# Optimization experiments

Hardware: AMD Instinct MI355X
Metric: run time of the kernel (lower is better)

Reference implementation:

```python
import jax, jax.numpy as jnp
import numpy as np

D = 1024   # model dim
H = 16     # heads
HD = D // H
L = 14     # layers
FF = 4096  # ffn hidden
T = 768    # sequence length


def layer_norm(x, g, b, eps):
    m = x.mean(-1, keepdims=True)
    v = ((x - m) ** 2).mean(-1, keepdims=True)
    return (x - m) / jnp.sqrt(v + eps) * g + b


def rel_pos_emb(t, d):
    # EspnetRelPositionalEncoding: concat(flip(pe_positive), pe_negative[1:]) -> (1, 2t-1, d)
    pos = jnp.arange(t, dtype=jnp.float32)
    div = jnp.exp(jnp.arange(0, d, 2, dtype=jnp.float32) * (-jnp.log(10000.0) / d))
    ang = pos[:, None] * div[None, :]                              # (t, d/2)
    pe_pos = jnp.stack([jnp.sin(ang), jnp.cos(ang)], -1).reshape(t, d)
    pe_neg = jnp.stack([jnp.sin(-ang), jnp.cos(-ang)], -1).reshape(t, d)
    return jnp.concatenate([pe_pos[::-1], pe_neg[1:]], 0)[None]    # (1, 2t-1, d)


def rel_shift(x):
    # x: (b, h, t, 2t-1) -> (b, h, t, t), Transformer-XL shift
    b, h, t, n = x.shape
    xp = jnp.concatenate([jnp.zeros((b, h, t, 1), x.dtype), x], -1)  # (b,h,t,n+1)
    xp = xp.reshape(b, h, n + 1, t)
    x = xp[:, :, 1:].reshape(b, h, t, n)
    return x[..., : n // 2 + 1]


def setup_inputs() -> dict:
    key = jax.random.key(0)
    ks = iter(jax.random.split(key, 40))
    s = 0.02
    nrm = lambda k, shape: jax.random.normal(k, shape, dtype=jnp.float32) * s
    return {
        "xs": jax.random.normal(next(ks), (1, T, D), dtype=jnp.float32),
        "embed_W": nrm(next(ks), (D, D)), "embed_b": jnp.zeros((D,), jnp.float32),
        "embed_ln_g": jnp.ones((D,), jnp.float32), "embed_ln_b": jnp.zeros((D,), jnp.float32),
        "Wq": nrm(next(ks), (L, D, D)), "bq": jnp.zeros((L, D), jnp.float32),
        "Wk": nrm(next(ks), (L, D, D)), "bk": jnp.zeros((L, D), jnp.float32),
        "Wv": nrm(next(ks), (L, D, D)), "bv": jnp.zeros((L, D), jnp.float32),
        "Wo": nrm(next(ks), (L, D, D)), "bo": jnp.zeros((L, D), jnp.float32),
        "Wp": nrm(next(ks), (L, D, D)),
        "pos_u": nrm(next(ks), (L, H, HD)), "pos_v": nrm(next(ks), (L, H, HD)),
        "ln1_g": jnp.ones((L, D), jnp.float32), "ln1_b": jnp.zeros((L, D), jnp.float32),
        "ln2_g": jnp.ones((L, D), jnp.float32), "ln2_b": jnp.zeros((L, D), jnp.float32),
        "ff_W1": nrm(next(ks), (L, D, FF)), "ff_b1": jnp.zeros((L, FF), jnp.float32),
        "ff_W2": nrm(next(ks), (L, FF, D)), "ff_b2": jnp.zeros((L, D), jnp.float32),
        "after_g": jnp.ones((D,), jnp.float32), "after_b": jnp.zeros((D,), jnp.float32),
    }


def reference(xs, embed_W, embed_b, embed_ln_g, embed_ln_b,
              Wq, bq, Wk, bk, Wv, bv, Wo, bo, Wp, pos_u, pos_v,
              ln1_g, ln1_b, ln2_g, ln2_b, ff_W1, ff_b1, ff_W2, ff_b2,
              after_g, after_b):
    b, t, _ = xs.shape
    # LegacyLinearNoSubsampling: Linear -> LayerNorm(eps=1e-5) -> (dropout) -> ReLU
    h = jnp.maximum(layer_norm(xs @ embed_W + embed_b, embed_ln_g, embed_ln_b, 1e-5), 0.0)
    x = h * jnp.sqrt(jnp.float32(D))          # pos-enc scale factor
    pos = rel_pos_emb(t, D)                    # (1, 2t-1, D)
    scale = jnp.float32(HD) ** -0.5
    for i in range(L):
        res = x
        xn = layer_norm(x, ln1_g[i], ln1_b[i], 1e-12)
        q = (xn @ Wq[i] + bq[i]).reshape(b, t, H, HD).transpose(0, 2, 1, 3)   # bhtd
        k = (xn @ Wk[i] + bk[i]).reshape(b, t, H, HD).transpose(0, 2, 1, 3)
        v = (xn @ Wv[i] + bv[i]).reshape(b, t, H, HD).transpose(0, 2, 1, 3)
        p = (pos @ Wp[i]).reshape(1, 2 * t - 1, H, HD).transpose(0, 2, 1, 3)  # bhnd
        ac = jnp.einsum('bhtd,bhsd->bhts', q + pos_u[i][None, :, None, :], k)
        bd = rel_shift(jnp.einsum('bhtd,bhnd->bhtn', q + pos_v[i][None, :, None, :], p))
        attn = jax.nn.softmax((ac + bd) * scale, axis=-1)
        o = jnp.einsum('bhts,bhsd->bhtd', attn, v).transpose(0, 2, 1, 3).reshape(b, t, D)
        x = res + (o @ Wo[i] + bo[i])
        res = x
        xn = layer_norm(x, ln2_g[i], ln2_b[i], 1e-12)
        x = res + (jnp.maximum(xn @ ff_W1[i] + ff_b1[i], 0.0) @ ff_W2[i] + ff_b2[i])
    return layer_norm(x, after_g, after_b, 1e-5)
```

## Files before the change

### kernel.cpp

```cpp
#include <hip/hip_runtime.h>
#include <hip/hip_bf16.h>
#include <math.h>

#define D_    1024
#define H_    16
#define HD_   64
#define L_    14
#define FF_   4096
#define T_    768
#define NPOS_ (2*T_-1)

using s16x8 = __attribute__((ext_vector_type(8))) short;
using f32x4 = __attribute__((ext_vector_type(4))) float;

__device__ inline short f2bf(float f) {
  __hip_bfloat16 h = __float2bfloat16(f);
  return *reinterpret_cast<short*>(&h);
}
__device__ inline float bf2f(unsigned short u) {
  union { unsigned u; float f; } v; v.u = ((unsigned)u) << 16; return v.f;
}

__device__ inline void gload_lds16(const unsigned short* g, short* lds) {
  __builtin_amdgcn_global_load_lds(
      (const __attribute__((address_space(1))) unsigned int*)g,
      (__attribute__((address_space(3))) unsigned int*)lds,
      16, 0, 0);
}

__device__ inline float waveRedSum(float v) {
#pragma unroll
  for (int o = 32; o > 0; o >>= 1) v += __shfl_down(v, o, 64);
  return v;
}
__device__ inline float blockRedSum(float v, float* sh) {
  int lane = threadIdx.x & 63, wid = threadIdx.x >> 6;
  v = waveRedSum(v);
  if (lane == 0) sh[wid] = v;
  __syncthreads();
  if (wid == 0) {
    float x = (lane < 4) ? sh[lane] : 0.f;
    x = waveRedSum(x);
    if (lane == 0) sh[0] = x;
  }
  __syncthreads();
  float r = sh[0];
  __syncthreads();
  return r;
}

__global__ __launch_bounds__(256) void ln_kernel(
    const float* __restrict__ x, const float* __restrict__ g,
    const float* __restrict__ b, void* __restrict__ y,
    float eps, int relu, float scale, int obf)
{
  __shared__ float sh[8];
  long row = blockIdx.x;
  const float* xr = x + row * D_;
  int tid = threadIdx.x;
  float4 v = *(const float4*)&xr[tid * 4];
  float s  = v.x + v.y + v.z + v.w;
  float sq = v.x * v.x + v.y * v.y + v.z * v.z + v.w * v.w;
  float mean = blockRedSum(s, sh) * (1.f / D_);
  float esq  = blockRedSum(sq, sh) * (1.f / D_);
  float var  = esq - mean * mean;
  if (var < 0.f) var = 0.f;
  float inv = rsqrtf(var + eps);
  float4 gv = *(const float4*)&g[tid * 4];
  float4 bv = *(const float4*)&b[tid * 4];
  float o0 = (v.x - mean) * inv * gv.x + bv.x;
  float o1 = (v.y - mean) * inv * gv.y + bv.y;
  float o2 = (v.z - mean) * inv * gv.z + bv.z;
  float o3 = (v.w - mean) * inv * gv.w + bv.w;
  if (relu) {
    o0 = fmaxf(o0, 0.f); o1 = fmaxf(o1, 0.f);
    o2 = fmaxf(o2, 0.f); o3 = fmaxf(o3, 0.f);
  }
  o0 *= scale; o1 *= scale; o2 *= scale; o3 *= scale;
  if (obf) {
    short4 sv;
    sv.x = f2bf(o0); sv.y = f2bf(o1); sv.z = f2bf(o2); sv.w = f2bf(o3);
    *(short4*)&((unsigned short*)y)[row * D_ + tid * 4] = sv;
  } else {
    float4 ov; ov.x = o0; ov.y = o1; ov.z = o2; ov.w = o3;
    *(float4*)&((float*)y)[row * D_ + tid * 4] = ov;
  }
}

__global__ __launch_bounds__(256) void transpose_kernel(
    const float* __restrict__ in, unsigned short* __restrict__ out, int K, int N)
{
  __shared__ unsigned short t[32][33];
  long z = blockIdx.z;
  in  += z * (long)K * N;
  out += z * (long)K * N;
  int n0 = blockIdx.x * 32, k0 = blockIdx.y * 32;
  int tid = threadIdx.x;
  int r = tid >> 3, c4 = (tid & 7) * 4;
  float4 v = *(const float4*)&in[(long)(k0 + r) * N + n0 + c4];
  t[r][c4 + 0] = (unsigned short)f2bf(v.x);
  t[r][c4 + 1] = (unsigned short)f2bf(v.y);
  t[r][c4 + 2] = (unsigned short)f2bf(v.z);
  t[r][c4 + 3] = (unsigned short)f2bf(v.w);
  __syncthreads();
  ushort4 s;
  s.x = t[c4 + 0][r]; s.y = t[c4 + 1][r]; s.z = t[c4 + 2][r]; s.w = t[c4 + 3][r];
  *(ushort4*)&out[(long)(n0 + r) * K + k0 + c4] = s;
}

template<int BM, int BN, int BMODE, bool CBF16>
__global__ __launch_bounds__(256) void gemm5_kernel(
    const unsigned short* __restrict__ A, int lda, long sAz,
    const void* __restrict__ B0, const void* __restrict__ B1, const void* __restrict__ B2,
    int ldb, long sBz,
    void* C0, void* C1, void* C2, int ldc, long sCz,
    const float* __restrict__ bias0, const float* __restrict__ bias1,
    const float* __restrict__ bias2,
    const float* __restrict__ resid, int ldres,
    int M, int N, int K, int zPerG, int relu, int nM)
{
  constexpr int FM = BM / 32, FN = BN / 32;
  constexpr int A_IT = BM / 32;
  constexpr int B_IT = BN / 32;
  constexpr int NSH = (BN == 128) ? 7 : 6;

  __shared__ short As[BM * 64];
  __shared__ short Bs[BN * 64];

  int nb = gridDim.x, bid = blockIdx.x;
  int q = nb >> 3, r = nb & 7, xcd = bid & 7, idx = bid >> 3;
  int lbid = (xcd < r ? xcd * (q + 1) : r * (q + 1) + (xcd - r) * q) + idx;
  int mT = lbid % nM, nT = lbid / nM;
  int m0 = mT * BM, n0 = nT * BN;

  int z = blockIdx.z;
  int g = z / zPerG, zb = z - g * zPerG;
  A += (long)zb * sAz;
  const void* Bv = (g == 0) ? B0 : ((g == 1) ? B1 : B2);
  void* Cv       = (g == 0) ? C0 : ((g == 1) ? C1 : C2);
  const float* bias = (g == 0) ? bias0 : ((g == 1) ? bias1 : bias2);
  const float* Bf = (const float*)Bv + zb * sBz;
  const unsigned short* Bh = (const unsigned short*)Bv + zb * sBz;
  float* Cf = (float*)Cv + zb * sCz;
  unsigned short* Ch = (unsigned short*)Cv + zb * sCz;

  int tid = threadIdx.x, lane = tid & 63, wid = tid >> 6;
  int wm0 = (wid >> 1) * (BM / 2), wn0 = (wid & 1) * (BN / 2);
  int lr = lane & 15, kl = (lane >> 4) * 8;

  f32x4 acc[FM][FN];
#pragma unroll
  for (int i = 0; i < FM; ++i)
#pragma unroll
    for (int j = 0; j < FN; ++j)
#pragma unroll
      for (int rr = 0; rr < 4; ++rr) acc[i][j][rr] = 0.f;

  for (int k0 = 0; k0 < K; k0 += 64) {
    if constexpr (BMODE == 1) {
      int lrow8 = lane >> 3;
      int lc8 = lane & 7;
#pragma unroll
      for (int it = 0; it < A_IT; ++it) {
        int row0 = (wid + it * 4) * 8;
        int row = row0 + lrow8;
        int gcol = lc8 ^ (row & 7);
        gload_lds16(A + (long)(m0 + row) * lda + k0 + gcol * 8, &As[row0 * 64]);
      }
#pragma unroll
      for (int it = 0; it < B_IT; ++it) {
        int row0 = (wid + it * 4) * 8;
        int row = row0 + lrow8;
        int gcol = lc8 ^ (row & 7);
        gload_lds16(Bh + (long)(n0 + row) * ldb + k0 + gcol * 8, &Bs[row0 * 64]);
      }
    } else {
#pragma unroll
      for (int it = 0; it < A_IT; ++it) {
        int f = tid + it * 256;
        int row = f >> 3, c8 = f & 7;
        int gm = m0 + row;
        s16x8 v = {0, 0, 0, 0, 0, 0, 0, 0};
        if (gm < M) v = *(const s16x8*)(A + (long)gm * lda + k0 + c8 * 8);
        *(s16x8*)&As[row * 64 + ((c8 ^ (row & 7)) << 3)] = v;
      }
      constexpr int B_IT2 = BN / 16;
#pragma unroll
      for (int it = 0; it < B_IT2; ++it) {
        int p = tid + it * 256;
        int n = p & (BN - 1), kq = p >> NSH;
        int gn = n0 + n;
        const float* bp = Bf + (long)(k0 + kq * 4) * ldb + gn;
        short4 s;
        s.x = f2bf(bp[0]); s.y = f2bf(bp[ldb]);
        s.z = f2bf(bp[2 * (long)ldb]); s.w = f2bf(bp[3 * (long)ldb]);
        *(short4*)&Bs[n * 64 + ((kq << 2) ^ ((n & 7) << 3))] = s;
      }
    }
    __syncthreads();
#pragma unroll
    for (int kk = 0; kk < 2; ++kk) {
      s16x8 a[FM], b[FN];
#pragma unroll
      for (int i = 0; i < FM; ++i) {
        int row = wm0 + i * 16 + lr;
        a[i] = *(const s16x8*)&As[row * 64 + ((kk * 32 + kl) ^ ((lr & 7) << 3))];
      }
#pragma unroll
      for (int j = 0; j < FN; ++j) {
        int row = wn0 + j * 16 + lr;
        b[j] = *(const s16x8*)&Bs[row * 64 + ((kk * 32 + kl) ^ ((lr & 7) << 3))];
      }
#pragma unroll
      for (int i = 0; i < FM; ++i)
#pragma unroll
        for (int j = 0; j < FN; ++j)
          acc[i][j] = __builtin_amdgcn_mfma_f32_16x16x32_bf16(a[i], b[j], acc[i][j], 0, 0, 0);
    }
    __syncthreads();
  }
#pragma unroll
  for (int i = 0; i < FM; ++i) {
#pragma unroll
    for (int j = 0; j < FN; ++j) {
      int n = n0 + wn0 + j * 16 + lr;
      float bv = bias ? bias[n] : 0.f;
#pragma unroll
      for (int rr = 0; rr < 4; ++rr) {
        int m = m0 + wm0 + i * 16 + (lane >> 4) * 4 + rr;
        if (m < M) {
          float v = acc[i][j][rr] + bv;
          if (resid) v += resid[(long)m * ldres + n];
          if (relu)  v = fmaxf(v, 0.f);
          if constexpr (CBF16) Ch[(long)m * ldc + n] = (unsigned short)f2bf(v);
          else                 Cf[(long)m * ldc + n] = v;
        }
      }
    }
  }
}

__global__ __launch_bounds__(256) void f2bf_kernel(
    const float* __restrict__ x, unsigned short* __restrict__ y, int n4)
{
  int i = blockIdx.x * 256 + threadIdx.x;
  if (i >= n4) return;
  float4 v = *(const float4*)&x[i * 4];
  short4 s; s.x = f2bf(v.x); s.y = f2bf(v.y); s.z = f2bf(v.z); s.w = f2bf(v.w);
  *(short4*)&y[i * 4] = s;
}

__global__ __launch_bounds__(256) void pos_kernel(unsigned short* __restrict__ pos)
{
  int idx = blockIdx.x * 256 + threadIdx.x;
  if (idx >= NPOS_ * (D_ / 2)) return;
  int n = idx / (D_ / 2), i = idx % (D_ / 2);
  float r = (float)(T_ - 1 - n);
  float div = __expf((float)(2 * i) * (-logf(10000.f) / (float)D_));
  float ang = r * div;
  pos[(long)n * D_ + 2 * i]     = (unsigned short)f2bf(sinf(ang));
  pos[(long)n * D_ + 2 * i + 1] = (unsigned short)f2bf(cosf(ang));
}

__global__ __launch_bounds__(256) void flash_attn_kernel(
    const unsigned short* __restrict__ Q, const unsigned short* __restrict__ K,
    const unsigned short* __restrict__ V, const unsigned short* __restrict__ P,
    const float* __restrict__ posu, const float* __restrict__ posv,
    unsigned short* __restrict__ O)
{
  __shared__ short Ks[64 * 64];
  __shared__ short Vs[64 * 64];
  __shared__ short Ps[96 * 64];
  __shared__ float Grgn[32 * 99];
  __shared__ float mxls[2][32], smls[2][32];

  short* qu = (short*)Grgn;
  short* qv = qu + 32 * 64;
  float* G  = Grgn;
  short* Pf = (short*)Grgn;

  int h = blockIdx.y;
  int t0 = blockIdx.x * 32;
  int tid = threadIdx.x, lane = tid & 63, w = tid >> 6;
  int wr = w >> 1, wc = w & 1;
  int lr = lane & 15, lg = lane >> 4;
  int kl = lg * 8;
  const float* pu = posu + h * HD_;
  const float* pv = posv + h * HD_;

  {
    int row = tid >> 3, c8 = tid & 7;
    s16x8 q8 = *(const s16x8*)(Q + (long)(t0 + row) * D_ + h * HD_ + c8 * 8);
    const unsigned short* qp = (const unsigned short*)&q8;
    s16x8 su, sv;
#pragma unroll
    for (int j = 0; j < 8; ++j) {
      float qf = bf2f(qp[j]);
      su[j] = f2bf(qf + pu[c8 * 8 + j]);
      sv[j] = f2bf(qf + pv[c8 * 8 + j]);
    }
    int sw = row * 64 + ((c8 ^ (row & 7)) << 3);
    *(s16x8*)&qu[sw] = su;
    *(s16x8*)&qv[sw] = sv;
  }
  __syncthreads();
  s16x8 aqu[2], aqv[2];
#pragma unroll
  for (int kk = 0; kk < 2; ++kk) {
    int row = wr * 16 + lr;
    int col = (kk * 32 + kl) ^ ((lr & 7) << 3);
    aqu[kk] = *(const s16x8*)&qu[row * 64 + col];
    aqv[kk] = *(const s16x8*)&qv[row * 64 + col];
  }

  float m_[4], l_[4];
  f32x4 acc_o[2];
#pragma unroll
  for (int rr = 0; rr < 4; ++rr) { m_[rr] = -1e30f; l_[rr] = 0.f; }
#pragma unroll
  for (int j = 0; j < 2; ++j)
#pragma unroll
    for (int rr = 0; rr < 4; ++rr) acc_o[j][rr] = 0.f;

  int lrow8 = lane >> 3, lc8 = lane & 7;

  for (int s0 = 0; s0 < T_; s0 += 64) {
    int base = s0 - t0 + T_ - 32;
    __syncthreads();
#pragma unroll
    for (int it = 0; it < 2; ++it) {
      int row0 = (w + it * 4) * 8;
      int row = row0 + lrow8;
      int gcol = lc8 ^ (row & 7);
      gload_lds16(K + (long)(s0 + row) * D_ + h * HD_ + gcol * 8, &Ks[row0 * 64]);
    }
#pragma unroll
    for (int it = 0; it < 4; ++it) {
      int d = tid & 63, sq = tid >> 6;
      int s = it * 16 + sq * 4;
      const unsigned short* vp = V + (long)(s0 + s) * D_ + h * HD_ + d;
      short4 sv4;
      sv4.x = (short)vp[0];
      sv4.y = (short)vp[D_];
      sv4.z = (short)vp[2 * D_];
      sv4.w = (short)vp[3 * D_];
      *(short4*)&Vs[d * 64 + (s ^ ((d & 7) << 3))] = sv4;
    }
#pragma unroll
    for (int it = 0; it < 3; ++it) {
      int row0 = (w + it * 4) * 8;
      int row = row0 + lrow8;
      int gp = base + row; if (gp > NPOS_ - 1) gp = NPOS_ - 1;
      int gcol = lc8 ^ (row & 7);
      gload_lds16(P + (long)gp * D_ + h * HD_ + gcol * 8, &Ps[row0 * 64]);
    }
    __syncthreads();
    f32x4 a_ac[2], a_g[3];
#pragma unroll
    for (int j = 0; j < 2; ++j)
#pragma unroll
      for (int rr = 0; rr < 4; ++rr) a_ac[j][rr] = 0.f;
#pragma unroll
    for (int j = 0; j < 3; ++j)
#pragma unroll
      for (int rr = 0; rr < 4; ++rr) a_g[j][rr] = 0.f;
#pragma unroll
    for (int j = 0; j < 2; ++j)
#pragma unroll
      for (int kk = 0; kk < 2; ++kk) {
        int row = wc * 32 + j * 16 + lr;
        s16x8 b = *(const s16x8*)&Ks[row * 64 + ((kk * 32 + kl) ^ ((lr & 7) << 3))];
        a_ac[j] = __builtin_amdgcn_mfma_f32_16x16x32_bf16(aqu[kk], b, a_ac[j], 0, 0, 0);
      }
#pragma unroll
    for (int j = 0; j < 3; ++j)
#pragma unroll
      for (int kk = 0; kk < 2; ++kk) {
        int row = wc * 48 + j * 16 + lr;
        s16x8 b = *(const s16x8*)&Ps[row * 64 + ((kk * 32 + kl) ^ ((lr & 7) << 3))];
        a_g[j] = __builtin_amdgcn_mfma_f32_16x16x32_bf16(aqv[kk], b, a_g[j], 0, 0, 0);
      }
#pragma unroll
    for (int j = 0; j < 3; ++j)
#pragma unroll
      for (int rr = 0; rr < 4; ++rr) {
        int row = wr * 16 + lg * 4 + rr;
        int col = wc * 48 + j * 16 + lr;
        G[row * 99 + col] = a_g[j][rr];
      }
    __syncthreads();
    float sreg[2][4], pm[4];
#pragma unroll
    for (int rr = 0; rr < 4; ++rr) {
      int row = wr * 16 + lg * 4 + rr;
#pragma unroll
      for (int j = 0; j < 2; ++j) {
        int c = wc * 32 + j * 16 + lr;
        int gc = c - row + 31;
        sreg[j][rr] = (a_ac[j][rr] + G[row * 99 + gc]) * 0.125f;
      }
      pm[rr] = fmaxf(sreg[0][rr], sreg[1][rr]);
    }
#pragma unroll
    for (int o = 1; o < 16; o <<= 1)
#pragma unroll
      for (int rr = 0; rr < 4; ++rr) pm[rr] = fmaxf(pm[rr], __shfl_xor(pm[rr], o, 64));
    if (lr == 0) {
#pragma unroll
      for (int rr = 0; rr < 4; ++rr) mxls[wc][wr * 16 + lg * 4 + rr] = pm[rr];
    }
    __syncthreads();
    float ps[4];
#pragma unroll
    for (int rr = 0; rr < 4; ++rr) {
      int row = wr * 16 + lg * 4 + rr;
      float mnew = fmaxf(m_[rr], fmaxf(mxls[0][row], mxls[1][row]));
      float sc = __expf(m_[rr] - mnew);
      m_[rr] = mnew;
      l_[rr] *= sc;
      acc_o[0][rr] *= sc;
      acc_o[1][rr] *= sc;
      float p0 = __expf(sreg[0][rr] - mnew);
      float p1 = __expf(sreg[1][rr] - mnew);
      ps[rr] = p0 + p1;
      int c0 = wc * 32 + lr, c1 = wc * 32 + 16 + lr;
      ((unsigned short*)Pf)[row * 64 + (c0 ^ ((row & 7) << 3))] = (unsigned short)f2bf(p0);
      ((unsigned short*)Pf)[row * 64 + (c1 ^ ((row & 7) << 3))] = (unsigned short)f2bf(p1);
    }
#pragma unroll
    for (int o = 1; o < 16; o <<= 1)
#pragma unroll
      for (int rr = 0; rr < 4; ++rr) ps[rr] += __shfl_xor(ps[rr], o, 64);
    if (lr == 0) {
#pragma unroll
      for (int rr = 0; rr < 4; ++rr) smls[wc][wr * 16 + lg * 4 + rr] = ps[rr];
    }
    __syncthreads();
#pragma unroll
    for (int rr = 0; rr < 4; ++rr) {
      int row = wr * 16 + lg * 4 + rr;
      l_[rr] += smls[0][row] + smls[1][row];
    }
    s16x8 ap[2];
#pragma unroll
    for (int kk = 0; kk < 2; ++kk) {
      int row = wr * 16 + lr;
      ap[kk] = *(const s16x8*)&((unsigned short*)Pf)[row * 64 + ((kk * 32 + kl) ^ ((lr & 7) << 3))];
    }
#pragma unroll
    for (int j = 0; j < 2; ++j)
#pragma unroll
      for (int kk = 0; kk < 2; ++kk) {
        int row = wc * 32 + j * 16 + lr;
        s16x8 b = *(const s16x8*)&Vs[row * 64 + ((kk * 32 + kl) ^ ((lr & 7) << 3))];
        acc_o[j] = __builtin_amdgcn_mfma_f32_16x16x32_bf16(ap[kk], b, acc_o[j], 0, 0, 0);
      }
  }
#pragma unroll
  for (int j = 0; j < 2; ++j)
#pragma unroll
    for (int rr = 0; rr < 4; ++rr) {
      int row = t0 + wr * 16 + lg * 4 + rr;
      int col = h * HD_ + wc * 32 + j * 16 + lr;
      O[(long)row * D_ + col] = (unsigned short)f2bf(acc_o[j][rr] / l_[rr]);
    }
}

extern "C" void kernel_launch(void* const* d_in, const int* in_sizes, int n_in,
                              void* d_out, int out_size, void* d_ws, size_t ws_size,
                              hipStream_t stream) {
  const float* xs       = (const float*)d_in[0];
  const float* embed_W  = (const float*)d_in[1];
  const float* embed_b  = (const float*)d_in[2];
  const float* embed_g  = (const float*)d_in[3];
  const float* embed_bt = (const float*)d_in[4];
  const float* Wq = (const float*)d_in[5];
  const float* bq = (const float*)d_in[6];
  const float* Wk = (const float*)d_in[7];
  const float* bk = (const float*)d_in[8];
  const float* Wv = (const float*)d_in[9];
  const float* bv = (const float*)d_in[10];
  const float* Wo = (const float*)d_in[11];
  const float* bo = (const float*)d_in[12];
  const float* Wp = (const float*)d_in[13];
  const float* pos_u = (const float*)d_in[14];
  const float* pos_v = (const float*)d_in[15];
  const float* ln1_g = (const float*)d_in[16];
  const float* ln1_b = (const float*)d_in[17];
  const float* ln2_g = (const float*)d_in[18];
  const float* ln2_b = (const float*)d_in[19];
  const float* ff_W1 = (const float*)d_in[20];
  const float* ff_b1 = (const float*)d_in[21];
  const float* ff_W2 = (const float*)d_in[22];
  const float* ff_b2 = (const float*)d_in[23];
  const float* after_g = (const float*)d_in[24];
  const float* after_b = (const float*)d_in[25];
  float* out = (float*)d_out;

  char* w = (char*)d_ws;
  auto carve = [&](size_t bytes) { char* p = w; w += (bytes + 255) & ~(size_t)255; return p; };
  float* bufX  = (float*)carve((size_t)T_ * D_ * 4);
  float* bufT  = (float*)carve((size_t)T_ * D_ * 4);
  unsigned short* xsb  = (unsigned short*)carve((size_t)T_ * D_ * 2);
  unsigned short* XNb  = (unsigned short*)carve((size_t)T_ * D_ * 2);
  unsigned short* Qb   = (unsigned short*)carve((size_t)T_ * D_ * 2);
  unsigned short* Kb   = (unsigned short*)carve((size_t)T_ * D_ * 2);
  unsigned short* Vb   = (unsigned short*)carve((size_t)T_ * D_ * 2);
  unsigned short* Ob   = (unsigned short*)carve((size_t)T_ * D_ * 2);
  unsigned short* Hb   = (unsigned short*)carve((size_t)T_ * FF_ * 2);
  unsigned short* posT = (unsigned short*)carve((size_t)(NPOS_ + 8) * D_ * 2);
  unsigned short* Pall = (unsigned short*)carve((size_t)L_ * NPOS_ * D_ * 2);
  size_t szDD = (size_t)D_ * D_;
  unsigned short* embedWt = (unsigned short*)carve(szDD * 2);
  unsigned short* WqT = (unsigned short*)carve((size_t)L_ * szDD * 2);
  unsigned short* WkT = (unsigned short*)carve((size_t)L_ * szDD * 2);
  unsigned short* WvT = (unsigned short*)carve((size_t)L_ * szDD * 2);
  unsigned short* WoT = (unsigned short*)carve((size_t)L_ * szDD * 2);
  unsigned short* WpT = (unsigned short*)carve((size_t)L_ * szDD * 2);
  unsigned short* W1T = (unsigned short*)carve((size_t)L_ * D_ * FF_ * 2);
  unsigned short* W2T = (unsigned short*)carve((size_t)L_ * D_ * FF_ * 2);
  bool fast = ((size_t)(w - (char*)d_ws) <= ws_size);

  {
    int n = NPOS_ * (D_ / 2);
    pos_kernel<<<(n + 255) / 256, 256, 0, stream>>>(posT);
  }
  f2bf_kernel<<<(T_ * D_ / 4 + 255) / 256, 256, 0, stream>>>(xs, xsb, T_ * D_ / 4);

  if (fast) {
    transpose_kernel<<<dim3(32, 32, 1),  256, 0, stream>>>(embed_W, embedWt, D_, D_);
    transpose_kernel<<<dim3(32, 32, L_), 256, 0, stream>>>(Wq, WqT, D_, D_);
    transpose_kernel<<<dim3(32, 32, L_), 256, 0, stream>>>(Wk, WkT, D_, D_);
    transpose_kernel<<<dim3(32, 32, L_), 256, 0, stream>>>(Wv, WvT, D_, D_);
    transpose_kernel<<<dim3(32, 32, L_), 256, 0, stream>>>(Wo, WoT, D_, D_);
    transpose_kernel<<<dim3(32, 32, L_), 256, 0, stream>>>(Wp, WpT, D_, D_);
    transpose_kernel<<<dim3(128, 32, L_), 256, 0, stream>>>(ff_W1, W1T, D_, FF_);
    transpose_kernel<<<dim3(32, 128, L_), 256, 0, stream>>>(ff_W2, W2T, FF_, D_);

    gemm5_kernel<32, 128, 1, false><<<dim3(192, 1, 1), 256, 0, stream>>>(
        xsb, D_, 0, embedWt, nullptr, nullptr, D_, 0,
        bufT, nullptr, nullptr, D_, 0, embed_b, nullptr, nullptr,
        nullptr, 0, T_, D_, D_, 1, 0, 24);
    ln_kernel<<<T_, 256, 0, stream>>>(bufT, embed_g, embed_bt, bufX, 1e-5f, 1, 32.0f, 0);

    gemm5_kernel<128, 64, 1, true><<<dim3(192, 1, 14), 256, 0, stream>>>(
        posT, D_, 0, WpT, nullptr, nullptr, D_, (long)szDD,
        Pall, nullptr, nullptr, D_, (long)NPOS_ * D_, nullptr, nullptr, nullptr,
        nullptr, 0, NPOS_, D_, D_, 14, 0, 12);

    for (int i = 0; i < L_; ++i) {
      ln_kernel<<<T_, 256, 0, stream>>>(bufX, ln1_g + (long)i * D_, ln1_b + (long)i * D_,
                                        XNb, 1e-12f, 0, 1.0f, 1);
      gemm5_kernel<32, 128, 1, true><<<dim3(192, 1, 3), 256, 0, stream>>>(
          XNb, D_, 0, WqT + i * szDD, WkT + i * szDD, WvT + i * szDD, D_, 0,
          Qb, Kb, Vb, D_, 0,
          bq + (long)i * D_, bk + (long)i * D_, bv + (long)i * D_,
          nullptr, 0, T_, D_, D_, 1, 0, 24);
      flash_attn_kernel<<<dim3(T_ / 32, H_), 256, 0, stream>>>(
          Qb, Kb, Vb, Pall + (long)i * NPOS_ * D_,
          pos_u + (long)i * D_, pos_v + (long)i * D_, Ob);
      gemm5_kernel<32, 64, 1, false><<<dim3(384, 1, 1), 256, 0, stream>>>(
          Ob, D_, 0, WoT + i * szDD, nullptr, nullptr, D_, 0,
          bufX, nullptr, nullptr, D_, 0, bo + (long)i * D_, nullptr, nullptr,
          bufX, D_, T_, D_, D_, 1, 0, 24);
      ln_kernel<<<T_, 256, 0, stream>>>(bufX, ln2_g + (long)i * D_, ln2_b + (long)i * D_,
                                        XNb, 1e-12f, 0, 1.0f, 1);
      gemm5_kernel<32, 128, 1, true><<<dim3(768, 1, 1), 256, 0, stream>>>(
          XNb, D_, 0, W1T + (size_t)i * D_ * FF_, nullptr, nullptr, D_, 0,
          Hb, nullptr, nullptr, FF_, 0, ff_b1 + (long)i * FF_, nullptr, nullptr,
          nullptr, 0, T_, FF_, D_, 1, 1, 24);
      gemm5_kernel<32, 64, 1, false><<<dim3(384, 1, 1), 256, 0, stream>>>(
          Hb, FF_, 0, W2T + (size_t)i * D_ * FF_, nullptr, nullptr, FF_, 0,
          bufX, nullptr, nullptr, D_, 0, ff_b2 + (long)i * D_, nullptr, nullptr,
          bufX, D_, T_, FF_, FF_, 1, 0, 24);
    }
  } else {
    gemm5_kernel<32, 128, 0, false><<<dim3(192, 1, 1), 256, 0, stream>>>(
        xsb, D_, 0, embed_W, nullptr, nullptr, D_, 0,
        bufT, nullptr, nullptr, D_, 0, embed_b, nullptr, nullptr,
        nullptr, 0, T_, D_, D_, 1, 0, 24);
    ln_kernel<<<T_, 256, 0, stream>>>(bufT, embed_g, embed_bt, bufX, 1e-5f, 1, 32.0f, 0);

    gemm5_kernel<128, 64, 0, true><<<dim3(192, 1, 14), 256, 0, stream>>>(
        posT, D_, 0, Wp, nullptr, nullptr, D_, (long)szDD,
        Pall, nullptr, nullptr, D_, (long)NPOS_ * D_, nullptr, nullptr, nullptr,
        nullptr, 0, NPOS_, D_, D_, 14, 0, 12);

    for (int i = 0; i < L_; ++i) {
      ln_kernel<<<T_, 256, 0, stream>>>(bufX, ln1_g + (long)i * D_, ln1_b + (long)i * D_,
                                        XNb, 1e-12f, 0, 1.0f, 1);
      gemm5_kernel<32, 128, 0, true><<<dim3(192, 1, 3), 256, 0, stream>>>(
          XNb, D_, 0, Wq + i * szDD, Wk + i * szDD, Wv + i * szDD, D_, 0,
          Qb, Kb, Vb, D_, 0,
          bq + (long)i * D_, bk + (long)i * D_, bv + (long)i * D_,
          nullptr, 0, T_, D_, D_, 1, 0, 24);
      flash_attn_kernel<<<dim3(T_ / 32, H_), 256, 0, stream>>>(
          Qb, Kb, Vb, Pall + (long)i * NPOS_ * D_,
          pos_u + (long)i * D_, pos_v + (long)i * D_, Ob);
      gemm5_kernel<32, 64, 0, false><<<dim3(384, 1, 1), 256, 0, stream>>>(
          Ob, D_, 0, Wo + i * szDD, nullptr, nullptr, D_, 0,
          bufX, nullptr, nullptr, D_, 0, bo + (long)i * D_, nullptr, nullptr,
          bufX, D_, T_, D_, D_, 1, 0, 24);
      ln_kernel<<<T_, 256, 0, stream>>>(bufX, ln2_g + (long)i * D_, ln2_b + (long)i * D_,
                                        XNb, 1e-12f, 0, 1.0f, 1);
      gemm5_kernel<32, 128, 0, true><<<dim3(768, 1, 1), 256, 0, stream>>>(
          XNb, D_, 0, ff_W1 + (size_t)i * D_ * FF_, nullptr, nullptr, FF_, 0,
          Hb, nullptr, nullptr, FF_, 0, ff_b1 + (long)i * FF_, nullptr, nullptr,
          nullptr, 0, T_, FF_, D_, 1, 1, 24);
      gemm5_kernel<32, 64, 0, false><<<dim3(384, 1, 1), 256, 0, stream>>>(
          Hb, FF_, 0, ff_W2 + (size_t)i * D_ * FF_, nullptr, nullptr, D_, 0,
          bufX, nullptr, nullptr, D_, 0, ff_b2 + (long)i * D_, nullptr, nullptr,
          bufX, D_, T_, FF_, FF_, 1, 0, 24);
    }
  }

  ln_kernel<<<T_, 256, 0, stream>>>(bufX, after_g, after_b, out, 1e-5f, 0, 1.0f, 0);
}
```

Before: 2.573 ms.

## Replace LDS-staged GEMM with direct-from-global register-fragment GEMM using 16-row tiles

Adds a gemm6 kernel that skips shared memory and barriers entirely. Each wave loads its MFMA A/B fragments straight from global memory into registers, and tiles are 16x128 per block. All fast-path GEMMs are switched to it with more blocks, and the LDS-async load mode is removed from gemm5. This aims to cut LDS traffic and sync overhead and to raise parallelism for the small-M GEMMs. The cost is that A fragments are re-read by all four waves and there is no cross-wave data reuse, so more load traffic goes to cache. The pos buffer padding is also increased.

```diff
diff --git a/kernel.cpp b/kernel.cpp
--- a/kernel.cpp
+++ b/kernel.cpp
@@ -108,7 +108,97 @@
   *(ushort4*)&out[(long)(n0 + r) * K + k0 + c4] = s;
 }
 
-template<int BM, int BN, int BMODE, bool CBF16>
+template<int BM, bool CBF16>
+__global__ __launch_bounds__(256) void gemm6_kernel(
+    const unsigned short* __restrict__ A, int lda, long sAz,
+    const unsigned short* __restrict__ B0, const unsigned short* __restrict__ B1,
+    const unsigned short* __restrict__ B2, int ldb, long sBz,
+    void* C0, void* C1, void* C2, int ldc, long sCz,
+    const float* __restrict__ bias0, const float* __restrict__ bias1,
+    const float* __restrict__ bias2,
+    const float* __restrict__ resid, int ldres,
+    int M, int N, int K, int zPerG, int relu, int nM)
+{
+  constexpr int FM = BM / 16;
+  constexpr int FN = 2;
+
+  int nb = gridDim.x, bid = blockIdx.x;
+  int q = nb >> 3, r = nb & 7, xcd = bid & 7, idx = bid >> 3;
+  int lbid = (xcd < r ? xcd * (q + 1) : r * (q + 1) + (xcd - r) * q) + idx;
+  int mT = lbid % nM, nT = lbid / nM;
+  int m0 = mT * BM, n0 = nT * 128;
+
+  int z = blockIdx.z;
+  int g = z / zPerG, zb = z - g * zPerG;
+  A += (long)zb * sAz;
+  const unsigned short* Bh = ((g == 0) ? B0 : ((g == 1) ? B1 : B2)) + zb * sBz;
+  void* Cv = (g == 0) ? C0 : ((g == 1) ? C1 : C2);
+  const float* bias = (g == 0) ? bias0 : ((g == 1) ? bias1 : bias2);
+  float* Cf = (float*)Cv + zb * sCz;
+  unsigned short* Ch = (unsigned short*)Cv + zb * sCz;
+
+  int tid = threadIdx.x, lane = tid & 63, wid = tid >> 6;
+  int wn0 = wid * 32;
+  int lr = lane & 15, kl = (lane >> 4) * 8;
+
+  const unsigned short* Ap[FM];
+  const unsigned short* Bp[FN];
+#pragma unroll
+  for (int i = 0; i < FM; ++i) Ap[i] = A + (long)(m0 + i * 16 + lr) * lda + kl;
+#pragma unroll
+  for (int j = 0; j < FN; ++j) Bp[j] = Bh + (long)(n0 + wn0 + j * 16 + lr) * ldb + kl;
+
+  f32x4 acc[FM][FN];
+#pragma unroll
+  for (int i = 0; i < FM; ++i)
+#pragma unroll
+    for (int j = 0; j < FN; ++j)
+#pragma unroll
+      for (int rr = 0; rr < 4; ++rr) acc[i][j][rr] = 0.f;
+
+  for (int k0 = 0; k0 < K; k0 += 64) {
+    s16x8 a[2][FM], b[2][FN];
+#pragma unroll
+    for (int kk = 0; kk < 2; ++kk) {
+#pragma unroll
+      for (int i = 0; i < FM; ++i) a[kk][i] = *(const s16x8*)(Ap[i] + kk * 32);
+#pragma unroll
+      for (int j = 0; j < FN; ++j) b[kk][j] = *(const s16x8*)(Bp[j] + kk * 32);
+    }
+#pragma unroll
+    for (int kk = 0; kk < 2; ++kk)
+#pragma unroll
+      for (int i = 0; i < FM; ++i)
+#pragma unroll
+        for (int j = 0; j < FN; ++j)
+          acc[i][j] = __builtin_amdgcn_mfma_f32_16x16x32_bf16(a[kk][i], b[kk][j], acc[i][j], 0, 0, 0);
+#pragma unroll
+    for (int i = 0; i < FM; ++i) Ap[i] += 64;
+#pragma unroll
+    for (int j = 0; j < FN; ++j) Bp[j] += 64;
+  }
+#pragma unroll
+  for (int i = 0; i < FM; ++i) {
+#pragma unroll
+    for (int j = 0; j < FN; ++j) {
+      int n = n0 + wn0 + j * 16 + lr;
+      float bv = bias ? bias[n] : 0.f;
+#pragma unroll
+      for (int rr = 0; rr < 4; ++rr) {
+        int m = m0 + i * 16 + (lane >> 4) * 4 + rr;
+        if (m < M) {
+          float v = acc[i][j][rr] + bv;
+          if (resid) v += resid[(long)m * ldres + n];
+          if (relu)  v = fmaxf(v, 0.f);
+          if constexpr (CBF16) Ch[(long)m * ldc + n] = (unsigned short)f2bf(v);
+          else                 Cf[(long)m * ldc + n] = v;
+        }
+      }
+    }
+  }
+}
+
+template<int BM, int BN, bool CBF16>
 __global__ __launch_bounds__(256) void gemm5_kernel(
     const unsigned short* __restrict__ A, int lda, long sAz,
     const void* __restrict__ B0, const void* __restrict__ B1, const void* __restrict__ B2,
@@ -121,7 +211,6 @@
 {
   constexpr int FM = BM / 32, FN = BN / 32;
   constexpr int A_IT = BM / 32;
-  constexpr int B_IT = BN / 32;
   constexpr int NSH = (BN == 128) ? 7 : 6;
 
   __shared__ short As[BM * 64];
@@ -140,7 +229,6 @@
   void* Cv       = (g == 0) ? C0 : ((g == 1) ? C1 : C2);
   const float* bias = (g == 0) ? bias0 : ((g == 1) ? bias1 : bias2);
   const float* Bf = (const float*)Bv + zb * sBz;
-  const unsigned short* Bh = (const unsigned short*)Bv + zb * sBz;
   float* Cf = (float*)Cv + zb * sCz;
   unsigned short* Ch = (unsigned short*)Cv + zb * sCz;
 
@@ -157,45 +245,26 @@
       for (int rr = 0; rr < 4; ++rr) acc[i][j][rr] = 0.f;
 
   for (int k0 = 0; k0 < K; k0 += 64) {
-    if constexpr (BMODE == 1) {
-      int lrow8 = lane >> 3;
-      int lc8 = lane & 7;
-#pragma unroll
-      for (int it = 0; it < A_IT; ++it) {
-        int row0 = (wid + it * 4) * 8;
-        int row = row0 + lrow8;
-        int gcol = lc8 ^ (row & 7);
-        gload_lds16(A + (long)(m0 + row) * lda + k0 + gcol * 8, &As[row0 * 64]);
-      }
-#pragma unroll
-      for (int it = 0; it < B_IT; ++it) {
-        int row0 = (wid + it * 4) * 8;
-        int row = row0 + lrow8;
-        int gcol = lc8 ^ (row & 7);
-        gload_lds16(Bh + (long)(n0 + row) * ldb + k0 + gcol * 8, &Bs[row0 * 64]);
-      }
-    } else {
-#pragma unroll
-      for (int it = 0; it < A_IT; ++it) {
-        int f = tid + it * 256;
-        int row = f >> 3, c8 = f & 7;
-        int gm = m0 + row;
-        s16x8 v = {0, 0, 0, 0, 0, 0, 0, 0};
-        if (gm < M) v = *(const s16x8*)(A + (long)gm * lda + k0 + c8 * 8);
-        *(s16x8*)&As[row * 64 + ((c8 ^ (row & 7)) << 3)] = v;
-      }
-      constexpr int B_IT2 = BN / 16;
-#pragma unroll
-      for (int it = 0; it < B_IT2; ++it) {
-        int p = tid + it * 256;
-        int n = p & (BN - 1), kq = p >> NSH;
-        int gn = n0 + n;
-        const float* bp = Bf + (long)(k0 + kq * 4) * ldb + gn;
-        short4 s;
-        s.x = f2bf(bp[0]); s.y = f2bf(bp[ldb]);
-        s.z = f2bf(bp[2 * (long)ldb]); s.w = f2bf(bp[3 * (long)ldb]);
-        *(short4*)&Bs[n * 64 + ((kq << 2) ^ ((n & 7) << 3))] = s;
-      }
+#pragma unroll
+    for (int it = 0; it < A_IT; ++it) {
+      int f = tid + it * 256;
+      int row = f >> 3, c8 = f & 7;
+      int gm = m0 + row;
+      s16x8 v = {0, 0, 0, 0, 0, 0, 0, 0};
+      if (gm < M) v = *(const s16x8*)(A + (long)gm * lda + k0 + c8 * 8);
+      *(s16x8*)&As[row * 64 + ((c8 ^ (row & 7)) << 3)] = v;
+    }
+    constexpr int B_IT2 = BN / 16;
+#pragma unroll
+    for (int it = 0; it < B_IT2; ++it) {
+      int p = tid + it * 256;
+      int n = p & (BN - 1), kq = p >> NSH;
+      int gn = n0 + n;
+      const float* bp = Bf + (long)(k0 + kq * 4) * ldb + gn;
+      short4 s;
+      s.x = f2bf(bp[0]); s.y = f2bf(bp[ldb]);
+      s.z = f2bf(bp[2 * (long)ldb]); s.w = f2bf(bp[3 * (long)ldb]);
+      *(short4*)&Bs[n * 64 + ((kq << 2) ^ ((n & 7) << 3))] = s;
     }
     __syncthreads();
 #pragma unroll
@@ -508,7 +577,7 @@
   unsigned short* Vb   = (unsigned short*)carve((size_t)T_ * D_ * 2);
   unsigned short* Ob   = (unsigned short*)carve((size_t)T_ * D_ * 2);
   unsigned short* Hb   = (unsigned short*)carve((size_t)T_ * FF_ * 2);
-  unsigned short* posT = (unsigned short*)carve((size_t)(NPOS_ + 8) * D_ * 2);
+  unsigned short* posT = (unsigned short*)carve((size_t)(NPOS_ + 16) * D_ * 2);
   unsigned short* Pall = (unsigned short*)carve((size_t)L_ * NPOS_ * D_ * 2);
   size_t szDD = (size_t)D_ * D_;
   unsigned short* embedWt = (unsigned short*)carve(szDD * 2);
@@ -537,51 +606,51 @@
     transpose_kernel<<<dim3(128, 32, L_), 256, 0, stream>>>(ff_W1, W1T, D_, FF_);
     transpose_kernel<<<dim3(32, 128, L_), 256, 0, stream>>>(ff_W2, W2T, FF_, D_);
 
-    gemm5_kernel<32, 128, 1, false><<<dim3(192, 1, 1), 256, 0, stream>>>(
+    gemm6_kernel<16, false><<<dim3(384, 1, 1), 256, 0, stream>>>(
         xsb, D_, 0, embedWt, nullptr, nullptr, D_, 0,
         bufT, nullptr, nullptr, D_, 0, embed_b, nullptr, nullptr,
-        nullptr, 0, T_, D_, D_, 1, 0, 24);
+        nullptr, 0, T_, D_, D_, 1, 0, 48);
     ln_kernel<<<T_, 256, 0, stream>>>(bufT, embed_g, embed_bt, bufX, 1e-5f, 1, 32.0f, 0);
 
-    gemm5_kernel<128, 64, 1, true><<<dim3(192, 1, 14), 256, 0, stream>>>(
+    gemm6_kernel<16, true><<<dim3(768, 1, 14), 256, 0, stream>>>(
         posT, D_, 0, WpT, nullptr, nullptr, D_, (long)szDD,
         Pall, nullptr, nullptr, D_, (long)NPOS_ * D_, nullptr, nullptr, nullptr,
-        nullptr, 0, NPOS_, D_, D_, 14, 0, 12);
+        nullptr, 0, NPOS_, D_, D_, 14, 0, 96);
 
     for (int i = 0; i < L_; ++i) {
       ln_kernel<<<T_, 256, 0, stream>>>(bufX, ln1_g + (long)i * D_, ln1_b + (long)i * D_,
                                         XNb, 1e-12f, 0, 1.0f, 1);
-      gemm5_kernel<32, 128, 1, true><<<dim3(192, 1, 3), 256, 0, stream>>>(
+      gemm6_kernel<16, true><<<dim3(384, 1, 3), 256, 0, stream>>>(
           XNb, D_, 0, WqT + i * szDD, WkT + i * szDD, WvT + i * szDD, D_, 0,
           Qb, Kb, Vb, D_, 0,
           bq + (long)i * D_, bk + (long)i * D_, bv + (long)i * D_,
-          nullptr, 0, T_, D_, D_, 1, 0, 24);
+          nullptr, 0, T_, D_, D_, 1, 0, 48);
       flash_attn_kernel<<<dim3(T_ / 32, H_), 256, 0, stream>>>(
           Qb, Kb, Vb, Pall + (long)i * NPOS_ * D_,
           pos_u + (long)i * D_, pos_v + (long)i * D_, Ob);
-      gemm5_kernel<32, 64, 1, false><<<dim3(384, 1, 1), 256, 0, stream>>>(
+      gemm6_kernel<16, false><<<dim3(384, 1, 1), 256, 0, stream>>>(
           Ob, D_, 0, WoT + i * szDD, nullptr, nullptr, D_, 0,
           bufX, nullptr, nullptr, D_, 0, bo + (long)i * D_, nullptr, nullptr,
-          bufX, D_, T_, D_, D_, 1, 0, 24);
+          bufX, D_, T_, D_, D_, 1, 0, 48);
       ln_kernel<<<T_, 256, 0, stream>>>(bufX, ln2_g + (long)i * D_, ln2_b + (long)i * D_,
                                         XNb, 1e-12f, 0, 1.0f, 1);
-      gemm5_kernel<32, 128, 1, true><<<dim3(768, 1, 1), 256, 0, stream>>>(
+      gemm6_kernel<16, true><<<dim3(1536, 1, 1), 256, 0, stream>>>(
           XNb, D_, 0, W1T + (size_t)i * D_ * FF_, nullptr, nullptr, D_, 0,
           Hb, nullptr, nullptr, FF_, 0, ff_b1 + (long)i * FF_, nullptr, nullptr,
-          nullptr, 0, T_, FF_, D_, 1, 1, 24);
-      gemm5_kernel<32, 64, 1, false><<<dim3(384, 1, 1), 256, 0, stream>>>(
+          nullptr, 0, T_, FF_, D_, 1, 1, 48);
+      gemm6_kernel<16, false><<<dim3(384, 1, 1), 256, 0, stream>>>(
           Hb, FF_, 0, W2T + (size_t)i * D_ * FF_, nullptr, nullptr, FF_, 0,
           bufX, nullptr, nullptr, D_, 0, ff_b2 + (long)i * D_, nullptr, nullptr,
-          bufX, D_, T_, FF_, FF_, 1, 0, 24);
+          bufX, D_, T_, FF_, FF_, 1, 0, 48);
     }
   } else {
-    gemm5_kernel<32, 128, 0, false><<<dim3(192, 1, 1), 256, 0, stream>>>(
+    gemm5_kernel<32, 128, false><<<dim3(192, 1, 1), 256, 0, stream>>>(
         xsb, D_, 0, embed_W, nullptr, nullptr, D_, 0,
         bufT, nullptr, nullptr, D_, 0, embed_b, nullptr, nullptr,
         nullptr, 0, T_, D_, D_, 1, 0, 24);
     ln_kernel<<<T_, 256, 0, stream>>>(bufT, embed_g, embed_bt, bufX, 1e-5f, 1, 32.0f, 0);
 
-    gemm5_kernel<128, 64, 0, true><<<dim3(192, 1, 14), 256, 0, stream>>>(
+    gemm5_kernel<128, 64, true><<<dim3(192, 1, 14), 256, 0, stream>>>(
         posT, D_, 0, Wp, nullptr, nullptr, D_, (long)szDD,
         Pall, nullptr, nullptr, D_, (long)NPOS_ * D_, nullptr, nullptr, nullptr,
         nullptr, 0, NPOS_, D_, D_, 14, 0, 12);
@@ -589,7 +658,7 @@
     for (int i = 0; i < L_; ++i) {
       ln_kernel<<<T_, 256, 0, stream>>>(bufX, ln1_g + (long)i * D_, ln1_b + (long)i * D_,
                                         XNb, 1e-12f, 0, 1.0f, 1);
-      gemm5_kernel<32, 128, 0, true><<<dim3(192, 1, 3), 256, 0, stream>>>(
+      gemm5_kernel<32, 128, true><<<dim3(192, 1, 3), 256, 0, stream>>>(
           XNb, D_, 0, Wq + i * szDD, Wk + i * szDD, Wv + i * szDD, D_, 0,
           Qb, Kb, Vb, D_, 0,
           bq + (long)i * D_, bk + (long)i * D_, bv + (long)i * D_,
@@ -597,17 +666,17 @@
       flash_attn_kernel<<<dim3(T_ / 32, H_), 256, 0, stream>>>(
           Qb, Kb, Vb, Pall + (long)i * NPOS_ * D_,
           pos_u + (long)i * D_, pos_v + (long)i * D_, Ob);
-      gemm5_kernel<32, 64, 0, false><<<dim3(384, 1, 1), 256, 0, stream>>>(
+      gemm5_kernel<32, 64, false><<<dim3(384, 1, 1), 256, 0, stream>>>(
           Ob, D_, 0, Wo + i * szDD, nullptr, nullptr, D_, 0,
           bufX, nullptr, nullptr, D_, 0, bo + (long)i * D_, nullptr, nullptr,
           bufX, D_, T_, D_, D_, 1, 0, 24);
       ln_kernel<<<T_, 256, 0, stream>>>(bufX, ln2_g + (long)i * D_, ln2_b + (long)i * D_,
                                         XNb, 1e-12f, 0, 1.0f, 1);
-      gemm5_kernel<32, 128, 0, true><<<dim3(768, 1, 1), 256, 0, stream>>>(
+      gemm5_kernel<32, 128, true><<<dim3(768, 1, 1), 256, 0, stream>>>(
           XNb, D_, 0, ff_W1 + (size_t)i * D_ * FF_, nullptr, nullptr, FF_, 0,
           Hb, nullptr, nullptr, FF_, 0, ff_b1 + (long)i * FF_, nullptr, nullptr,
           nullptr, 0, T_, FF_, D_, 1, 1, 24);
-      gemm5_kernel<32, 64, 0, false><<<dim3(384, 1, 1), 256, 0, stream>>>(
+      gemm5_kernel<32, 64, false><<<dim3(384, 1, 1), 256, 0, stream>>>(
           Hb, FF_, 0, ff_W2 + (size_t)i * D_ * FF_, nullptr, nullptr, D_, 0,
           bufX, nullptr, nullptr, D_, 0, ff_b2 + (long)i * D_, nullptr, nullptr,
           bufX, D_, T_, FF_, FF_, 1, 0, 24);
```

Measured after the change: 4.626 ms. 1.8x slower.
